# Kernel optimization log

Hardware: AMD Instinct MI355X
Metric: run time of the kernel (lower is better)

## Reference

```python
import jax, jax.numpy as jnp
import numpy as np

N = 50000      # nodes
E = 800000     # edges
F_IN = 128     # input node feature dim
H = 4          # attention heads
DH = 64        # per-head hidden dim
HID = H * DH   # 256
NEG_SLOPE = 0.2


def gat_conv(h, src, dst, W, al, ar, b, res):
    # DGL GATConv: project, compute attention logits, edge softmax over dst, aggregate.
    feat = (h @ W).reshape(N, H, DH)                      # [N,H,DH]
    el = jnp.einsum('nhd,hd->nh', feat, al)               # [N,H]
    er = jnp.einsum('nhd,hd->nh', feat, ar)               # [N,H]
    e = el[src] + er[dst]                                 # [E,H]
    e = jnp.where(e > 0, e, NEG_SLOPE * e)                # LeakyReLU(0.2)
    m = jax.ops.segment_max(e, dst, num_segments=N)       # [N,H]
    m = jnp.where(jnp.isfinite(m), m, 0.0)                # zero-in-degree safety
    ex = jnp.exp(e - m[dst])                              # [E,H]
    denom = jax.ops.segment_sum(ex, dst, num_segments=N)  # [N,H]
    alpha = ex / jnp.maximum(denom[dst], 1e-16)           # edge softmax
    out = jax.ops.segment_sum(feat[src] * alpha[:, :, None], dst, num_segments=N)
    return out + res.reshape(N, H, DH) + b.reshape(1, H, DH)


def setup_inputs() -> dict:
    key = jax.random.key(0)
    ks = jax.random.split(key, 16)
    x = jax.random.normal(ks[0], (N, F_IN), jnp.float32)
    edge_index = jax.random.randint(ks[1], (2, E), 0, N)
    s_in = 1.0 / np.sqrt(F_IN)
    s_h = 1.0 / np.sqrt(HID)
    W0 = jax.random.normal(ks[2], (F_IN, HID), jnp.float32) * s_in
    W1 = jax.random.normal(ks[3], (HID, HID), jnp.float32) * s_h
    W2 = jax.random.normal(ks[4], (HID, HID), jnp.float32) * s_h
    al0 = jax.random.normal(ks[5], (H, DH), jnp.float32) * 0.1
    al1 = jax.random.normal(ks[6], (H, DH), jnp.float32) * 0.1
    al2 = jax.random.normal(ks[7], (H, DH), jnp.float32) * 0.1
    ar0 = jax.random.normal(ks[8], (H, DH), jnp.float32) * 0.1
    ar1 = jax.random.normal(ks[9], (H, DH), jnp.float32) * 0.1
    ar2 = jax.random.normal(ks[10], (H, DH), jnp.float32) * 0.1
    b0 = jnp.zeros((HID,), jnp.float32)
    b1 = jnp.zeros((HID,), jnp.float32)
    b2 = jnp.zeros((HID,), jnp.float32)
    resW0 = jax.random.normal(ks[11], (F_IN, HID), jnp.float32) * s_in
    return {"x": x, "edge_index": edge_index,
            "W0": W0, "W1": W1, "W2": W2,
            "al0": al0, "al1": al1, "al2": al2,
            "ar0": ar0, "ar1": ar1, "ar2": ar2,
            "b0": b0, "b1": b1, "b2": b2,
            "resW0": resW0}


def reference(x, edge_index, W0, W1, W2, al0, al1, al2, ar0, ar1, ar2, b0, b1, b2, resW0):
    src, dst = edge_index[0], edge_index[1]
    # layer 0: residual via linear projection (in != heads*hidden)
    h = gat_conv(x, src, dst, W0, al0, ar0, b0, x @ resW0).reshape(N, HID)
    h = jax.nn.relu(h)
    # layer 1: identity residual
    h = gat_conv(h, src, dst, W1, al1, ar1, b1, h).reshape(N, HID)
    h = jax.nn.relu(h)
    # layer 2: identity residual, mean over heads
    h = gat_conv(h, src, dst, W2, al2, ar2, b2, h)
    return h.mean(axis=1)  # [N, DH]
```

## Files before the change

### kernel.cpp

```cpp
#include <hip/hip_runtime.h>
#include <math.h>

#define N_NODES 50000
#define N_EDGES 800000
#define F_INPUT 128
#define HEADS 4
#define DHID 64
#define HID 256
#define M_PAD 50048
#define SCAN_B 49

typedef _Float16 half8 __attribute__((ext_vector_type(8)));
typedef _Float16 half4 __attribute__((ext_vector_type(4)));
typedef float f32x4 __attribute__((ext_vector_type(4)));


#define EB_BLOCKS ((N_EDGES + 255) / 256)
#define PREP_A 1600000
#define PREP_B (PREP_A + 196608)
#define PREP_C (PREP_B + 10240)
#define PB_BLOCKS ((PREP_C + 255) / 256)

__global__ void hist_prep_kernel(const int* __restrict__ dst, int* __restrict__ counts,
                                 int* __restrict__ rank,
                                 const float* __restrict__ x, _Float16* __restrict__ x16,
                                 const float* __restrict__ W0, const float* __restrict__ WR,
                                 _Float16* __restrict__ WtL0,
                                 const float* __restrict__ W1, _Float16* __restrict__ Wt1,
                                 const float* __restrict__ W2, _Float16* __restrict__ Wt2,
                                 const float* __restrict__ al0, const float* __restrict__ ar0,
                                 const float* __restrict__ al1, const float* __restrict__ ar1,
                                 const float* __restrict__ al2, const float* __restrict__ ar2) {
    if (blockIdx.x < EB_BLOCKS) {
        int e = blockIdx.x * 256 + threadIdx.x;
        if (e < N_EDGES) rank[e] = atomicAdd(&counts[dst[e]], 1);
        return;
    }
    int t = (blockIdx.x - EB_BLOCKS) * 256 + threadIdx.x;
    if (t < PREP_A) {
        f32x4 v = *(const f32x4*)&x[t * 4];
        half4 h = {(_Float16)v.x, (_Float16)v.y, (_Float16)v.z, (_Float16)v.w};
        *(half4*)&x16[(size_t)t * 4] = h;
    } else if (t < PREP_B) {
        int u = t - PREP_A;
        if (u < 65536) {
            int c = u >> 7;
            int k = u & 127;
            float v = (c < 256) ? W0[k * 256 + c] : WR[k * 256 + (c - 256)];
            WtL0[u] = (_Float16)v;
        } else if (u < 131072) {
            int w = u - 65536;
            int c = w >> 8;
            int k = w & 255;
            Wt1[w] = (_Float16)W1[k * 256 + c];
        } else {
            int w = u - 131072;
            int c = w >> 8;
            int k = w & 255;
            Wt2[w] = (_Float16)W2[k * 256 + c];
        }
    } else if (t < PREP_C) {
        int u = t - PREP_B;
        if (u < 2048) {
            int row8 = u >> 7, k = u & 127;
            int h = row8 & 3;
            const float* vec = (row8 < 4) ? al0 : ar0;
            float s = 0.f;
            for (int d = 0; d < 64; d++) s += W0[k * 256 + h * 64 + d] * vec[h * 64 + d];
            WtL0[(512 + row8) * 128 + k] = (_Float16)s;
        } else if (u < 6144) {
            int w = u - 2048;
            int row8 = w >> 8, k = w & 255;
            int h = row8 & 3;
            const float* vec = (row8 < 4) ? al1 : ar1;
            float s = 0.f;
            for (int d = 0; d < 64; d++) s += W1[k * 256 + h * 64 + d] * vec[h * 64 + d];
            Wt1[(256 + row8) * 256 + k] = (_Float16)s;
        } else {
            int w = u - 6144;
            int row8 = w >> 8, k = w & 255;
            int h = row8 & 3;
            const float* vec = (row8 < 4) ? al2 : ar2;
            float s = 0.f;
            for (int d = 0; d < 64; d++) s += W2[k * 256 + h * 64 + d] * vec[h * 64 + d];
            Wt2[(256 + row8) * 256 + k] = (_Float16)s;
        }
    }
}


__global__ __launch_bounds__(256) void scan1_kernel(const int* __restrict__ counts,
                                                    int* __restrict__ pre,
                                                    int* __restrict__ bsum) {
    __shared__ int buf[256];
    int tid = threadIdx.x;
    int idx = blockIdx.x * 1024 + tid * 4;
    int v0 = 0, v1 = 0, v2 = 0, v3 = 0;
    if (idx + 3 < N_NODES) {
        int4 v = *(const int4*)&counts[idx];
        v0 = v.x; v1 = v.y; v2 = v.z; v3 = v.w;
    } else {
        if (idx + 0 < N_NODES) v0 = counts[idx + 0];
        if (idx + 1 < N_NODES) v1 = counts[idx + 1];
        if (idx + 2 < N_NODES) v2 = counts[idx + 2];
    }
    int s0 = v0, s1 = s0 + v1, s2 = s1 + v2, s3 = s2 + v3;
    buf[tid] = s3;
    __syncthreads();
    for (int off = 1; off < 256; off <<= 1) {
        int t = (tid >= off) ? buf[tid - off] : 0;
        __syncthreads();
        buf[tid] += t;
        __syncthreads();
    }
    int excl = buf[tid] - s3;
    if (idx + 0 < N_NODES) pre[idx + 0] = excl + s0;
    if (idx + 1 < N_NODES) pre[idx + 1] = excl + s1;
    if (idx + 2 < N_NODES) pre[idx + 2] = excl + s2;
    if (idx + 3 < N_NODES) pre[idx + 3] = excl + s3;
    if (tid == 255) bsum[blockIdx.x] = buf[255];
}

__global__ __launch_bounds__(256) void scan23_kernel(const int* __restrict__ pre,
                                                     const int* __restrict__ bsum,
                                                     int* __restrict__ row_ptr) {
    __shared__ int bq[64];
    int tid = threadIdx.x;
    if (tid < 64) {
        int v = (tid < SCAN_B) ? bsum[tid] : 0;
        int orig = v;
#pragma unroll
        for (int off = 1; off < 64; off <<= 1) {
            int t = __shfl_up(v, off, 64);
            if (tid >= off) v += t;
        }
        bq[tid] = v - orig;
    }
    __syncthreads();
    int add = bq[blockIdx.x];
    int idx = blockIdx.x * 1024 + tid * 4;
#pragma unroll
    for (int u = 0; u < 4; u++) {
        int i = idx + u;
        if (i < N_NODES) row_ptr[i + 1] = pre[i] + add;
    }
    if (blockIdx.x == 0 && tid == 0) row_ptr[0] = 0;
}


__device__ __forceinline__ void gl2lds16(const void* g, void* l) {
    __builtin_amdgcn_global_load_lds((const __attribute__((address_space(1))) void*)g,
                                     (__attribute__((address_space(3))) void*)l, 16, 0, 0);
}


#define SC_B ((N_EDGES + 511) / 512)
#define GB0 (M_PAD / 64)

__global__ __launch_bounds__(512) void scat_gemm0_kernel(
        const int* __restrict__ src, const int* __restrict__ dst,
        const int* __restrict__ row_ptr, const int* __restrict__ rank,
        int* __restrict__ esrc,
        const _Float16* __restrict__ A16, const _Float16* __restrict__ WtL0,
        _Float16* __restrict__ feat16, _Float16* __restrict__ res16,
        float* __restrict__ el, float* __restrict__ er) {
    if (blockIdx.x < SC_B) {
        int e = blockIdx.x * 512 + threadIdx.x;
        if (e < N_EDGES) {
            int d = dst[e];
            esrc[row_ptr[d] + rank[e]] = src[e];
        }
        return;
    }
    __shared__ __align__(16) _Float16 As[4 * 512];
    __shared__ __align__(16) _Float16 Ws[33 * 512];
    int tid = threadIdx.x;
    int w = tid >> 6;
    int lane = tid & 63;
    int lrow = lane & 15;
    int lk = lane >> 4;
    int row0 = (blockIdx.x - SC_B) * 64;

    f32x4 acc[4][4] = {};
    f32x4 acc5[4] = {};

    for (int k0 = 0; k0 < F_INPUT; k0 += 32) {
        if (w < 4)
            gl2lds16(A16 + (size_t)(row0 + w * 16 + lrow) * F_INPUT + k0 + lk * 8, &As[w * 512]);
#pragma unroll
        for (int i = 0; i < 4; i++) {
            int tt = i * 8 + w;
            gl2lds16(WtL0 + (size_t)(tt * 16 + lrow) * F_INPUT + k0 + lk * 8, &Ws[tt * 512]);
        }
        if (w == 7)
            gl2lds16(WtL0 + (size_t)(512 + lrow) * F_INPUT + k0 + lk * 8, &Ws[32 * 512]);
        __syncthreads();
        half8 a[4], b[4], b5;
#pragma unroll
        for (int m = 0; m < 4; m++) a[m] = *(const half8*)&As[m * 512 + lane * 8];
#pragma unroll
        for (int j = 0; j < 4; j++) b[j] = *(const half8*)&Ws[(w * 4 + j) * 512 + lane * 8];
        if (w == 3) b5 = *(const half8*)&Ws[32 * 512 + lane * 8];
#pragma unroll
        for (int m = 0; m < 4; m++)
#pragma unroll
            for (int j = 0; j < 4; j++)
                acc[m][j] = __builtin_amdgcn_mfma_f32_16x16x32_f16(a[m], b[j], acc[m][j], 0, 0, 0);
        if (w == 3) {
#pragma unroll
            for (int m = 0; m < 4; m++)
                acc5[m] = __builtin_amdgcn_mfma_f32_16x16x32_f16(a[m], b5, acc5[m], 0, 0, 0);
        }
        __syncthreads();
    }

    if (w < 4) {
#pragma unroll
        for (int m = 0; m < 4; m++) {
#pragma unroll
            for (int r = 0; r < 4; r++) {
                int row = row0 + m * 16 + lk * 4 + r;
                if (row < N_NODES) {
#pragma unroll
                    for (int j = 0; j < 4; j++)
                        feat16[(size_t)row * HID + w * 64 + j * 16 + lrow] = (_Float16)acc[m][j][r];
                }
            }
        }
        if (w == 3 && lrow < 8) {
#pragma unroll
            for (int m = 0; m < 4; m++) {
#pragma unroll
                for (int r = 0; r < 4; r++) {
                    int row = row0 + m * 16 + lk * 4 + r;
                    if (row < N_NODES) {
                        float v = acc5[m][r];
                        if (lrow < 4) el[row * 4 + lrow] = v;
                        else          er[row * 4 + (lrow - 4)] = v;
                    }
                }
            }
        }
    } else {
        int wc = w - 4;
#pragma unroll
        for (int m = 0; m < 4; m++) {
#pragma unroll
            for (int r = 0; r < 4; r++) {
                int row = row0 + m * 16 + lk * 4 + r;
                if (row < N_NODES) {
#pragma unroll
                    for (int j = 0; j < 4; j++)
                        res16[(size_t)row * HID + wc * 64 + j * 16 + lrow] = (_Float16)acc[m][j][r];
                }
            }
        }
    }
}

__global__ __launch_bounds__(512) void gemm_h(const _Float16* __restrict__ A16,
                                              const _Float16* __restrict__ Wt,
                                              _Float16* __restrict__ feat16,
                                              float* __restrict__ el, float* __restrict__ er) {
    __shared__ __align__(16) _Float16 As[8 * 2 * 512];
    __shared__ __align__(16) _Float16 Ws[17 * 2 * 512];
    int tid = threadIdx.x;
    int w = tid >> 6;
    int lane = tid & 63;
    int lrow = lane & 15;
    int lk = lane >> 4;
    int wrow = w >> 2;
    int wcol = w & 3;
    int row0 = blockIdx.x * 128;

    f32x4 acc[4][4] = {};
    f32x4 acc5[4] = {};

    for (int k0 = 0; k0 < HID; k0 += 64) {
#pragma unroll
        for (int c = 0; c < 2; c++) {
            int kk = k0 + c * 32 + lk * 8;
            gl2lds16(A16 + (size_t)(row0 + w * 16 + lrow) * HID + kk, &As[(w * 2 + c) * 512]);
            gl2lds16(Wt + (size_t)(w * 16 + lrow) * HID + kk, &Ws[(w * 2 + c) * 512]);
            gl2lds16(Wt + (size_t)((w + 8) * 16 + lrow) * HID + kk, &Ws[((w + 8) * 2 + c) * 512]);
            if (w == 0)
                gl2lds16(Wt + (size_t)(256 + lrow) * HID + kk, &Ws[(16 * 2 + c) * 512]);
        }
        __syncthreads();
#pragma unroll
        for (int c = 0; c < 2; c++) {
            half8 a[4], b[4], b5;
#pragma unroll
            for (int m = 0; m < 4; m++)
                a[m] = *(const half8*)&As[((wrow * 4 + m) * 2 + c) * 512 + lane * 8];
#pragma unroll
            for (int j = 0; j < 4; j++)
                b[j] = *(const half8*)&Ws[((wcol * 4 + j) * 2 + c) * 512 + lane * 8];
            if (wcol == 3) b5 = *(const half8*)&Ws[(16 * 2 + c) * 512 + lane * 8];
#pragma unroll
            for (int m = 0; m < 4; m++)
#pragma unroll
                for (int j = 0; j < 4; j++)
                    acc[m][j] = __builtin_amdgcn_mfma_f32_16x16x32_f16(a[m], b[j], acc[m][j], 0, 0, 0);
            if (wcol == 3) {
#pragma unroll
                for (int m = 0; m < 4; m++)
                    acc5[m] = __builtin_amdgcn_mfma_f32_16x16x32_f16(a[m], b5, acc5[m], 0, 0, 0);
            }
        }
        __syncthreads();
    }

#pragma unroll
    for (int m = 0; m < 4; m++) {
#pragma unroll
        for (int r = 0; r < 4; r++) {
            int row = row0 + wrow * 64 + m * 16 + lk * 4 + r;
            if (row < N_NODES) {
#pragma unroll
                for (int j = 0; j < 4; j++)
                    feat16[(size_t)row * HID + wcol * 64 + j * 16 + lrow] = (_Float16)acc[m][j][r];
            }
        }
    }
    if (wcol == 3 && lrow < 8) {
#pragma unroll
        for (int m = 0; m < 4; m++) {
#pragma unroll
            for (int r = 0; r < 4; r++) {
                int row = row0 + wrow * 64 + m * 16 + lk * 4 + r;
                if (row < N_NODES) {
                    float v = acc5[m][r];
                    if (lrow < 4) el[row * 4 + lrow] = v;
                    else          er[row * 4 + (lrow - 4)] = v;
                }
            }
        }
    }
}


__global__ __launch_bounds__(256) void agg_kernel(const _Float16* __restrict__ feat16,
                                                  const float* __restrict__ el,
                                                  const float* __restrict__ er,
                                                  const int* __restrict__ row_ptr,
                                                  const int* __restrict__ esrc,
                                                  const _Float16* __restrict__ res16,
                                                  const float* __restrict__ bias,
                                                  _Float16* __restrict__ out16,
                                                  float* __restrict__ outmean,
                                                  int do_relu) {
    __shared__ float lds[4][4 * 65 + 64];
    int wv = threadIdx.x >> 6;
    int lane = threadIdx.x & 63;
    int n = blockIdx.x * 4 + wv;
    int li = lane & 31;
    int sub = lane >> 5;
    int head = li >> 3;
    int start = row_ptr[n];
    int deg = row_ptr[n + 1] - start;
    f32x4 ern = *(const f32x4*)&er[n * 4];
    float* L = lds[wv];
    float* Loff = L + 4 * 65;
    const float* Lex = L + head * 65;

    f32x4 accA = {0.f, 0.f, 0.f, 0.f};
    f32x4 accB = {0.f, 0.f, 0.f, 0.f};
    f32x4 sm4 = {0.f, 0.f, 0.f, 0.f};
    const char* fbase = (const char*)feat16 + li * 16;

    for (int base = 0; base < deg; base += 64) {
        int e = base + lane;
        f32x4 ex4 = {0.f, 0.f, 0.f, 0.f};
        int off = 0;
        if (e < deg) {
            int s = esrc[start + e];
            off = s * (HID * 2);
            f32x4 v = *(const f32x4*)&el[s * 4];
            v = v + ern;
            v.x = v.x > 0.f ? v.x : 0.2f * v.x;
            v.y = v.y > 0.f ? v.y : 0.2f * v.y;
            v.z = v.z > 0.f ? v.z : 0.2f * v.z;
            v.w = v.w > 0.f ? v.w : 0.2f * v.w;
            ex4.x = __expf(v.x);
            ex4.y = __expf(v.y);
            ex4.z = __expf(v.z);
            ex4.w = __expf(v.w);
        }
        L[0 * 65 + lane] = ex4.x;
        L[1 * 65 + lane] = ex4.y;
        L[2 * 65 + lane] = ex4.z;
        L[3 * 65 + lane] = ex4.w;
        Loff[lane] = __int_as_float(off);
        sm4 += ex4;

        int cnt = min(64, deg - base);
        int cnt16 = (cnt + 15) & ~15;
        for (int j = 0; j < cnt16; j += 16) {
            float ex[8]; int o[8];
#pragma unroll
            for (int u = 0; u < 8; u++) {
                int e2 = j + u * 2 + sub;
                ex[u] = Lex[e2];
                o[u] = __float_as_int(Loff[e2]);
            }
            half8 f[8];
#pragma unroll
            for (int u = 0; u < 8; u++) f[u] = *(const half8*)(fbase + o[u]);
#pragma unroll
            for (int u = 0; u < 8; u++) {
                accA.x += ex[u] * (float)f[u][0];
                accA.y += ex[u] * (float)f[u][1];
                accA.z += ex[u] * (float)f[u][2];
                accA.w += ex[u] * (float)f[u][3];
                accB.x += ex[u] * (float)f[u][4];
                accB.y += ex[u] * (float)f[u][5];
                accB.z += ex[u] * (float)f[u][6];
                accB.w += ex[u] * (float)f[u][7];
            }
        }
    }

    accA.x += __shfl_xor(accA.x, 32, 64);
    accA.y += __shfl_xor(accA.y, 32, 64);
    accA.z += __shfl_xor(accA.z, 32, 64);
    accA.w += __shfl_xor(accA.w, 32, 64);
    accB.x += __shfl_xor(accB.x, 32, 64);
    accB.y += __shfl_xor(accB.y, 32, 64);
    accB.z += __shfl_xor(accB.z, 32, 64);
    accB.w += __shfl_xor(accB.w, 32, 64);

#pragma unroll
    for (int off2 = 1; off2 < 64; off2 <<= 1) {
        sm4.x += __shfl_xor(sm4.x, off2, 64);
        sm4.y += __shfl_xor(sm4.y, off2, 64);
        sm4.z += __shfl_xor(sm4.z, off2, 64);
        sm4.w += __shfl_xor(sm4.w, off2, 64);
    }
    float smh = (head == 0) ? sm4.x : (head == 1) ? sm4.y : (head == 2) ? sm4.z : sm4.w;
    float inv = 1.f / fmaxf(smh, 1e-16f);
    accA *= inv;
    accB *= inv;

    half8 rv = *(const half8*)&res16[(size_t)n * HID + li * 8];
    f32x4 bvA = *(const f32x4*)&bias[li * 8];
    f32x4 bvB = *(const f32x4*)&bias[li * 8 + 4];
    accA.x += (float)rv[0] + bvA.x;
    accA.y += (float)rv[1] + bvA.y;
    accA.z += (float)rv[2] + bvA.z;
    accA.w += (float)rv[3] + bvA.w;
    accB.x += (float)rv[4] + bvB.x;
    accB.y += (float)rv[5] + bvB.y;
    accB.z += (float)rv[6] + bvB.z;
    accB.w += (float)rv[7] + bvB.w;
    if (do_relu) {
        accA.x = fmaxf(accA.x, 0.f); accA.y = fmaxf(accA.y, 0.f);
        accA.z = fmaxf(accA.z, 0.f); accA.w = fmaxf(accA.w, 0.f);
        accB.x = fmaxf(accB.x, 0.f); accB.y = fmaxf(accB.y, 0.f);
        accB.z = fmaxf(accB.z, 0.f); accB.w = fmaxf(accB.w, 0.f);
    }
    if (outmean) {
#pragma unroll
        for (int st = 8; st <= 16; st <<= 1) {
            accA.x += __shfl_xor(accA.x, st, 64);
            accA.y += __shfl_xor(accA.y, st, 64);
            accA.z += __shfl_xor(accA.z, st, 64);
            accA.w += __shfl_xor(accA.w, st, 64);
            accB.x += __shfl_xor(accB.x, st, 64);
            accB.y += __shfl_xor(accB.y, st, 64);
            accB.z += __shfl_xor(accB.z, st, 64);
            accB.w += __shfl_xor(accB.w, st, 64);
        }
        if (sub == 0 && li < 8) {
            f32x4 moA = accA * 0.25f;
            f32x4 moB = accB * 0.25f;
            *(f32x4*)&outmean[(size_t)n * DHID + li * 8] = moA;
            *(f32x4*)&outmean[(size_t)n * DHID + li * 8 + 4] = moB;
        }
    } else {
        if (sub == 0) {
            half8 h = {(_Float16)accA.x, (_Float16)accA.y, (_Float16)accA.z, (_Float16)accA.w,
                       (_Float16)accB.x, (_Float16)accB.y, (_Float16)accB.z, (_Float16)accB.w};
            *(half8*)&out16[(size_t)n * HID + li * 8] = h;
        }
    }
}


extern "C" void kernel_launch(void* const* d_in, const int* in_sizes, int n_in,
                              void* d_out, int out_size, void* d_ws, size_t ws_size,
                              hipStream_t stream) {
    const float* x     = (const float*)d_in[0];
    const int*   ei    = (const int*)d_in[1];
    const float* W0    = (const float*)d_in[2];
    const float* W1    = (const float*)d_in[3];
    const float* W2    = (const float*)d_in[4];
    const float* al0   = (const float*)d_in[5];
    const float* al1   = (const float*)d_in[6];
    const float* al2   = (const float*)d_in[7];
    const float* ar0   = (const float*)d_in[8];
    const float* ar1   = (const float*)d_in[9];
    const float* ar2   = (const float*)d_in[10];
    const float* b0    = (const float*)d_in[11];
    const float* b1    = (const float*)d_in[12];
    const float* b2    = (const float*)d_in[13];
    const float* resW0 = (const float*)d_in[14];
    float* out = (float*)d_out;

    const int* srcp = ei;
    const int* dstp = ei + N_EDGES;

    char* p = (char*)d_ws;
    auto alloc = [&](size_t bytes) -> char* {
        char* r = p;
        p += (bytes + 255) & ~(size_t)255;
        return r;
    };
    _Float16*  h16    = (_Float16*)alloc((size_t)M_PAD * HID * 2);
    _Float16*  feat16 = (_Float16*)alloc((size_t)M_PAD * HID * 2);
    _Float16*  res0   = (_Float16*)alloc((size_t)N_NODES * HID * 2);
    _Float16*  x16    = (_Float16*)alloc((size_t)M_PAD * F_INPUT * 2);
    float*     el     = (float*)alloc((size_t)N_NODES * HEADS * 4);
    float*     er     = (float*)alloc((size_t)N_NODES * HEADS * 4);
    _Float16*  WtL0   = (_Float16*)alloc((size_t)528 * F_INPUT * 2);
    _Float16*  Wt1    = (_Float16*)alloc((size_t)272 * HID * 2);
    _Float16*  Wt2    = (_Float16*)alloc((size_t)272 * HID * 2);
    int*       counts = (int*)alloc((size_t)N_NODES * 4);
    int*       rank   = (int*)alloc((size_t)N_EDGES * 4);
    int*       rowptr = (int*)alloc((size_t)(N_NODES + 1) * 4);
    int*       esrc   = (int*)alloc((size_t)N_EDGES * 4);
    int*       pre    = (int*)alloc((size_t)N_NODES * 4);
    int*       bsum   = (int*)alloc((size_t)SCAN_B * 4);

    const int NB = N_NODES / 4;

    hipMemsetAsync(counts, 0, (size_t)N_NODES * 4, stream);
    hist_prep_kernel<<<EB_BLOCKS + PB_BLOCKS, 256, 0, stream>>>(
        dstp, counts, rank, x, x16, W0, resW0, WtL0, W1, Wt1, W2, Wt2,
        al0, ar0, al1, ar1, al2, ar2);
    scan1_kernel<<<SCAN_B, 256, 0, stream>>>(counts, pre, bsum);
    scan23_kernel<<<SCAN_B, 256, 0, stream>>>(pre, bsum, rowptr);

    scat_gemm0_kernel<<<SC_B + GB0, 512, 0, stream>>>(
        srcp, dstp, rowptr, rank, esrc, x16, WtL0, feat16, res0, el, er);
    agg_kernel<<<NB, 256, 0, stream>>>(feat16, el, er, rowptr, esrc, res0, b0, h16, nullptr, 1);

    gemm_h<<<M_PAD / 128, 512, 0, stream>>>(h16, Wt1, feat16, el, er);
    agg_kernel<<<NB, 256, 0, stream>>>(feat16, el, er, rowptr, esrc, h16, b1, h16, nullptr, 1);

    gemm_h<<<M_PAD / 128, 512, 0, stream>>>(h16, Wt2, feat16, el, er);
    agg_kernel<<<NB, 256, 0, stream>>>(feat16, el, er, rowptr, esrc, h16, b2, nullptr, out, 0);
}
```

Baseline: 446.6 us.

## Load GEMM fragments directly from global memory with register double-buffering

Both projection GEMMs (layer-0 fused scatter+GEMM and the hidden-layer GEMM) no longer stage A and W tiles through LDS with global_load_lds and barriers. Each wave now reads its MFMA fragments straight from global memory and prefetches the next K-slice into registers while the current MFMAs run. This removes LDS traffic and __syncthreads, but loses sharing across waves, so W and A rows are re-read by several waves through cache. It also raises register pressure.

```diff
diff --git a/kernel.cpp b/kernel.cpp
--- a/kernel.cpp
+++ b/kernel.cpp
@@ -148,12 +148,6 @@
 }
 
 
-__device__ __forceinline__ void gl2lds16(const void* g, void* l) {
-    __builtin_amdgcn_global_load_lds((const __attribute__((address_space(1))) void*)g,
-                                     (__attribute__((address_space(3))) void*)l, 16, 0, 0);
-}
-
-
 #define SC_B ((N_EDGES + 511) / 512)
 #define GB0 (M_PAD / 64)
 
@@ -172,8 +166,6 @@
         }
         return;
     }
-    __shared__ __align__(16) _Float16 As[4 * 512];
-    __shared__ __align__(16) _Float16 Ws[33 * 512];
     int tid = threadIdx.x;
     int w = tid >> 6;
     int lane = tid & 63;
@@ -183,35 +175,49 @@
 
     f32x4 acc[4][4] = {};
     f32x4 acc5[4] = {};
+    bool do5 = (w == 3);
+
+    const _Float16* Arow[4];
+#pragma unroll
+    for (int m = 0; m < 4; m++)
+        Arow[m] = A16 + (size_t)(row0 + m * 16 + lrow) * F_INPUT + lk * 8;
+    const _Float16* Brow[4];
+#pragma unroll
+    for (int j = 0; j < 4; j++)
+        Brow[j] = WtL0 + (size_t)((w * 4 + j) * 16 + lrow) * F_INPUT + lk * 8;
+    const _Float16* B5row = WtL0 + (size_t)(512 + lrow) * F_INPUT + lk * 8;
+
+    half8 a[4], b[4], b5;
+#pragma unroll
+    for (int m = 0; m < 4; m++) a[m] = *(const half8*)(Arow[m]);
+#pragma unroll
+    for (int j = 0; j < 4; j++) b[j] = *(const half8*)(Brow[j]);
+    if (do5) b5 = *(const half8*)(B5row);
 
     for (int k0 = 0; k0 < F_INPUT; k0 += 32) {
-        if (w < 4)
-            gl2lds16(A16 + (size_t)(row0 + w * 16 + lrow) * F_INPUT + k0 + lk * 8, &As[w * 512]);
-#pragma unroll
-        for (int i = 0; i < 4; i++) {
-            int tt = i * 8 + w;
-            gl2lds16(WtL0 + (size_t)(tt * 16 + lrow) * F_INPUT + k0 + lk * 8, &Ws[tt * 512]);
-        }
-        if (w == 7)
-            gl2lds16(WtL0 + (size_t)(512 + lrow) * F_INPUT + k0 + lk * 8, &Ws[32 * 512]);
-        __syncthreads();
-        half8 a[4], b[4], b5;
-#pragma unroll
-        for (int m = 0; m < 4; m++) a[m] = *(const half8*)&As[m * 512 + lane * 8];
-#pragma unroll
-        for (int j = 0; j < 4; j++) b[j] = *(const half8*)&Ws[(w * 4 + j) * 512 + lane * 8];
-        if (w == 3) b5 = *(const half8*)&Ws[32 * 512 + lane * 8];
+        half8 an[4], bn[4], b5n;
+        if (k0 + 32 < F_INPUT) {
+#pragma unroll
+            for (int m = 0; m < 4; m++) an[m] = *(const half8*)(Arow[m] + k0 + 32);
+#pragma unroll
+            for (int j = 0; j < 4; j++) bn[j] = *(const half8*)(Brow[j] + k0 + 32);
+            if (do5) b5n = *(const half8*)(B5row + k0 + 32);
+        }
 #pragma unroll
         for (int m = 0; m < 4; m++)
 #pragma unroll
             for (int j = 0; j < 4; j++)
                 acc[m][j] = __builtin_amdgcn_mfma_f32_16x16x32_f16(a[m], b[j], acc[m][j], 0, 0, 0);
-        if (w == 3) {
+        if (do5) {
 #pragma unroll
             for (int m = 0; m < 4; m++)
                 acc5[m] = __builtin_amdgcn_mfma_f32_16x16x32_f16(a[m], b5, acc5[m], 0, 0, 0);
         }
-        __syncthreads();
+#pragma unroll
+        for (int m = 0; m < 4; m++) a[m] = an[m];
+#pragma unroll
+        for (int j = 0; j < 4; j++) b[j] = bn[j];
+        if (do5) b5 = b5n;
     }
 
     if (w < 4) {
@@ -262,8 +268,6 @@
                                               const _Float16* __restrict__ Wt,
                                               _Float16* __restrict__ feat16,
                                               float* __restrict__ el, float* __restrict__ er) {
-    __shared__ __align__(16) _Float16 As[8 * 2 * 512];
-    __shared__ __align__(16) _Float16 Ws[17 * 2 * 512];
     int tid = threadIdx.x;
     int w = tid >> 6;
     int lane = tid & 63;
@@ -275,40 +279,49 @@
 
     f32x4 acc[4][4] = {};
     f32x4 acc5[4] = {};
-
-    for (int k0 = 0; k0 < HID; k0 += 64) {
-#pragma unroll
-        for (int c = 0; c < 2; c++) {
-            int kk = k0 + c * 32 + lk * 8;
-            gl2lds16(A16 + (size_t)(row0 + w * 16 + lrow) * HID + kk, &As[(w * 2 + c) * 512]);
-            gl2lds16(Wt + (size_t)(w * 16 + lrow) * HID + kk, &Ws[(w * 2 + c) * 512]);
-            gl2lds16(Wt + (size_t)((w + 8) * 16 + lrow) * HID + kk, &Ws[((w + 8) * 2 + c) * 512]);
-            if (w == 0)
-                gl2lds16(Wt + (size_t)(256 + lrow) * HID + kk, &Ws[(16 * 2 + c) * 512]);
-        }
-        __syncthreads();
-#pragma unroll
-        for (int c = 0; c < 2; c++) {
-            half8 a[4], b[4], b5;
+    bool do5 = (wcol == 3);
+
+    const _Float16* Arow[4];
+#pragma unroll
+    for (int m = 0; m < 4; m++)
+        Arow[m] = A16 + (size_t)(row0 + wrow * 64 + m * 16 + lrow) * HID + lk * 8;
+    const _Float16* Brow[4];
+#pragma unroll
+    for (int j = 0; j < 4; j++)
+        Brow[j] = Wt + (size_t)(wcol * 64 + j * 16 + lrow) * HID + lk * 8;
+    const _Float16* B5row = Wt + (size_t)(256 + lrow) * HID + lk * 8;
+
+    half8 a[4], b[4], b5;
+#pragma unroll
+    for (int m = 0; m < 4; m++) a[m] = *(const half8*)(Arow[m]);
+#pragma unroll
+    for (int j = 0; j < 4; j++) b[j] = *(const half8*)(Brow[j]);
+    if (do5) b5 = *(const half8*)(B5row);
+
+    for (int k0 = 0; k0 < HID; k0 += 32) {
+        half8 an[4], bn[4], b5n;
+        if (k0 + 32 < HID) {
+#pragma unroll
+            for (int m = 0; m < 4; m++) an[m] = *(const half8*)(Arow[m] + k0 + 32);
+#pragma unroll
+            for (int j = 0; j < 4; j++) bn[j] = *(const half8*)(Brow[j] + k0 + 32);
+            if (do5) b5n = *(const half8*)(B5row + k0 + 32);
+        }
+#pragma unroll
+        for (int m = 0; m < 4; m++)
+#pragma unroll
+            for (int j = 0; j < 4; j++)
+                acc[m][j] = __builtin_amdgcn_mfma_f32_16x16x32_f16(a[m], b[j], acc[m][j], 0, 0, 0);
+        if (do5) {
 #pragma unroll
             for (int m = 0; m < 4; m++)
-                a[m] = *(const half8*)&As[((wrow * 4 + m) * 2 + c) * 512 + lane * 8];
-#pragma unroll
-            for (int j = 0; j < 4; j++)
-                b[j] = *(const half8*)&Ws[((wcol * 4 + j) * 2 + c) * 512 + lane * 8];
-            if (wcol == 3) b5 = *(const half8*)&Ws[(16 * 2 + c) * 512 + lane * 8];
-#pragma unroll
-            for (int m = 0; m < 4; m++)
-#pragma unroll
-                for (int j = 0; j < 4; j++)
-                    acc[m][j] = __builtin_amdgcn_mfma_f32_16x16x32_f16(a[m], b[j], acc[m][j], 0, 0, 0);
-            if (wcol == 3) {
-#pragma unroll
-                for (int m = 0; m < 4; m++)
-                    acc5[m] = __builtin_amdgcn_mfma_f32_16x16x32_f16(a[m], b5, acc5[m], 0, 0, 0);
-            }
-        }
-        __syncthreads();
+                acc5[m] = __builtin_amdgcn_mfma_f32_16x16x32_f16(a[m], b5, acc5[m], 0, 0, 0);
+        }
+#pragma unroll
+        for (int m = 0; m < 4; m++) a[m] = an[m];
+#pragma unroll
+        for (int j = 0; j < 4; j++) b[j] = bn[j];
+        if (do5) b5 = b5n;
     }
 
 #pragma unroll
```

Result: slower. 468.9 us (+5.0%).
